# Performance work log

Measured on AMD Instinct MI355X. Metric: run time of the kernel, lower is better.

## Reference

```python
import jax, jax.numpy as jnp
import numpy as np

B, S, C = 4, 4096, 1024   # batch, input_size (seq len), channels
H, D, DK = 16, 64, 256    # nhead, head dim, dim_k (Linformer projection)


def setup_inputs() -> dict:
    key = jax.random.key(0)
    ks = jax.random.split(key, 9)
    s_in = 1.0 / np.sqrt(C)
    s_e = 1.0 / np.sqrt(S)
    return {
        'x':   jax.random.normal(ks[0], (B, S, C), jnp.float32),
        # per-head Q/K/V projection weights (Linear(channels, dim, bias=False))
        'Wq':  jax.random.normal(ks[1], (H, D, C), jnp.float32) * s_in,
        'Wk':  jax.random.normal(ks[2], (H, D, C), jnp.float32) * s_in,
        'Wv':  jax.random.normal(ks[3], (H, D, C), jnp.float32) * s_in,
        # shared (layerwise) E/F Linear(input_size, dim_k) with bias
        'E_w': jax.random.normal(ks[4], (DK, S), jnp.float32) * s_e,
        'E_b': jnp.zeros((DK,), jnp.float32),
        'F_w': jax.random.normal(ks[5], (DK, S), jnp.float32) * s_e,
        'F_b': jnp.zeros((DK,), jnp.float32),
        # output projection Linear(dim*nhead, channels)
        'Wo':  jax.random.normal(ks[6], (C, H * D), jnp.float32) * (1.0 / np.sqrt(H * D)),
        'bo':  jnp.zeros((C,), jnp.float32),
    }


def reference(x, Wq, Wk, Wv, E_w, E_b, F_w, F_b, Wo, bo):
    b, s, c = x.shape
    h, d, _ = Wq.shape
    # per-head projections (vectorized over the Python head loop)
    Q = jnp.einsum('bsc,hdc->bhsd', x, Wq)            # [B,H,S,D]
    Kt = jnp.einsum('bsc,hdc->bhds', x, Wk)           # K already transposed: [B,H,D,S]
    Vt = jnp.einsum('bsc,hdc->bhds', x, Wv)           # [B,H,D,S]
    # Linformer low-rank projections along the sequence axis
    Kp = jnp.einsum('bhds,ks->bhdk', Kt, E_w) + E_b   # [B,H,D,DK]
    Vp = jnp.einsum('bhds,ks->bhdk', Vt, F_w) + F_b   # [B,H,D,DK]
    scores = jnp.einsum('bhsd,bhdk->bhsk', Q, Kp) / jnp.sqrt(jnp.asarray(d, x.dtype))
    P = jax.nn.softmax(scores, axis=-1)               # softmax over projected dim_k
    head_out = jnp.einsum('bhsk,bhdk->bhsd', P, Vp)   # [B,H,S,D]
    out = head_out.transpose(0, 2, 1, 3).reshape(b, s, h * d)  # concat heads
    return out @ Wo.T + bo
```

## Files before the change

kernel.cpp:

```cpp
#include <hip/hip_runtime.h>
#include <stdint.h>

typedef __attribute__((ext_vector_type(8))) short bf16x8;
typedef __attribute__((ext_vector_type(4))) float f32x4;
typedef __attribute__((ext_vector_type(16))) float f32x16;

__device__ __forceinline__ unsigned short f2b(float f) {
  union { float f; uint32_t u; } v; v.f = f;
  uint32_t u = v.u;
  return (unsigned short)((u + 0x7FFFu + ((u >> 16) & 1u)) >> 16);
}

__device__ __forceinline__ void gll16(const unsigned short* gsrc, unsigned short* lds_uniform) {
  __builtin_amdgcn_global_load_lds(
      (const __attribute__((address_space(1))) uint32_t*)gsrc,
      (__attribute__((address_space(3))) uint32_t*)lds_uniform,
      16, 0, 0);
}

#define MFMA(a, b, c) __builtin_amdgcn_mfma_f32_16x16x32_bf16((a), (b), (c), 0, 0, 0)
#define MFMA32(a, b, c) __builtin_amdgcn_mfma_f32_32x32x16_bf16((a), (b), (c), 0, 0, 0)

__global__ void cast_x_dual(const float* __restrict__ x,
                            unsigned short* __restrict__ xb,
                            unsigned short* __restrict__ xT) {
  __shared__ unsigned short tile[64][65];
  const int st = blockIdx.x * 64;
  const int ct = blockIdx.y * 64;
  const int b = blockIdx.z;
  const int t = threadIdx.x;
#pragma unroll
  for (int it = 0; it < 4; ++it) {
    int linear = (it * 256 + t) * 4;
    int r = linear >> 6, c = linear & 63;
    float4 v = *(const float4*)(x + ((size_t)(b * 4096 + st + r)) * 1024 + ct + c);
    ushort4 o;
    o.x = f2b(v.x); o.y = f2b(v.y); o.z = f2b(v.z); o.w = f2b(v.w);
    *(ushort4*)(xb + ((size_t)(b * 4096 + st + r)) * 1024 + ct + c) = o;
    tile[r][c] = o.x; tile[r][c + 1] = o.y; tile[r][c + 2] = o.z; tile[r][c + 3] = o.w;
  }
  __syncthreads();
#pragma unroll
  for (int it = 0; it < 4; ++it) {
    int linear = (it * 256 + t) * 4;
    int r = linear >> 6, c = linear & 63;
    ushort4 o;
    o.x = tile[c][r]; o.y = tile[c + 1][r]; o.z = tile[c + 2][r]; o.w = tile[c + 3][r];
    *(ushort4*)(xT + ((size_t)b * 1024 + ct + r) * 4096 + st + c) = o;
  }
}

__global__ void cast6(const float* __restrict__ s0, const float* __restrict__ s1,
                      const float* __restrict__ s2, const float* __restrict__ s3,
                      const float* __restrict__ s4, const float* __restrict__ s5,
                      const float* __restrict__ E_b, const float* __restrict__ F_b,
                      unsigned short* __restrict__ d0, unsigned short* __restrict__ d1,
                      unsigned short* __restrict__ d2, unsigned short* __restrict__ d3,
                      unsigned short* __restrict__ d4, unsigned short* __restrict__ d5,
                      float* __restrict__ EFbias) {
  if (blockIdx.y == 6) {
    if (blockIdx.x == 0) {
      int t = threadIdx.x;
      EFbias[t] = E_b[t];
      EFbias[256 + t] = F_b[t];
    }
    return;
  }
  const float* src; unsigned short* dst; float sc = 1.0f;
  switch (blockIdx.y) {
    case 0: src = s0; dst = d0; sc = 0.18033688011112042f; break;
    case 1: src = s1; dst = d1; break;
    case 2: src = s2; dst = d2; break;
    case 3: src = s3; dst = d3; break;
    case 4: src = s4; dst = d4; break;
    default: src = s5; dst = d5; break;
  }
  int i = (blockIdx.x * 256 + threadIdx.x) * 4;
  float4 v = *(const float4*)(src + i);
  ushort4 o;
  o.x = f2b(v.x * sc); o.y = f2b(v.y * sc); o.z = f2b(v.z * sc); o.w = f2b(v.w * sc);
  *(ushort4*)(dst + i) = o;
}

template <int BIAS, bool OBF16>
__global__ __launch_bounds__(512, 2) void gemm_bt256(
    const unsigned short* __restrict__ A, const unsigned short* __restrict__ B,
    void* __restrict__ Cout, const float* __restrict__ bias,
    int K, int lda, int ldb, int ldc) {
  __shared__ unsigned short Asm_[2][2][256 * 32];
  __shared__ unsigned short Bsm_[2][2][256 * 32];
  const int tid = threadIdx.x;
  const int wave = tid >> 6, lane = tid & 63;
  const int g = (lane >> 4) & 3, l15 = lane & 15;
  const int wmi = wave >> 2, wni = wave & 3;
  const int bm = blockIdx.x * 256, bn = blockIdx.y * 256;

  const int rc = lane >> 2;

#define STG256(XA, H, J, T, BUF)                                              \
  {                                                                           \
    int k2_ = wave * 2 + (J);                                                 \
    int p_ = k2_ >> 3, cc_ = k2_ & 7;                                         \
    int rr_ = (H) * 128 + cc_ * 16 + rc;                                      \
    int sl_ = (lane & 3) ^ ((rr_ >> 1) & 3);                                  \
    const unsigned short* s_ = (XA)                                           \
        ? A + (size_t)(bm + rr_) * lda + (T) * 64 + p_ * 32 + sl_ * 8         \
        : B + (size_t)(bn + rr_) * ldb + (T) * 64 + p_ * 32 + sl_ * 8;        \
    unsigned short* d_ = ((XA) ? &Asm_[BUF][p_][0] : &Bsm_[BUF][p_][0])       \
                         + ((H) * 128 + cc_ * 16) * 32;                       \
    gll16(s_, d_);                                                            \
  }

  f32x4 acc[8][4];
#pragma unroll
  for (int i = 0; i < 8; ++i)
#pragma unroll
    for (int j = 0; j < 4; ++j) acc[i][j] = (f32x4){0.f, 0.f, 0.f, 0.f};

  const int nt = K >> 6;
  STG256(1, 0, 0, 0, 0) STG256(1, 0, 1, 0, 0)
  STG256(0, 0, 0, 0, 0) STG256(0, 0, 1, 0, 0)
  STG256(1, 1, 0, 0, 0) STG256(1, 1, 1, 0, 0)
  STG256(0, 1, 0, 0, 0) STG256(0, 1, 1, 0, 0)
  asm volatile("s_waitcnt vmcnt(0)" ::: "memory");
  __builtin_amdgcn_s_barrier();
  asm volatile("" ::: "memory");

  for (int t = 0; t < nt; ++t) {
    const int cur = t & 1, nxt = cur ^ 1;
    const char* Ap0 = (const char*)&Asm_[cur][0][0];
    const char* Ap1 = (const char*)&Asm_[cur][1][0];
    const char* Bp0 = (const char*)&Bsm_[cur][0][0];
    const char* Bp1 = (const char*)&Bsm_[cur][1][0];
    const bool more = (t + 1 < nt);

    bf16x8 bf[4][2];
#pragma unroll
    for (int ni = 0; ni < 4; ++ni) {
      int n = wni * 64 + ni * 16 + l15;
      int sw = ((g ^ ((n >> 1) & 3)) << 4);
      bf[ni][0] = *(const bf16x8*)(Bp0 + n * 64 + sw);
      bf[ni][1] = *(const bf16x8*)(Bp1 + n * 64 + sw);
    }

#pragma unroll
    for (int q = 0; q < 4; ++q) {
      if (q == 0 && more) {
        STG256(1, 0, 0, t + 1, nxt) STG256(1, 0, 1, t + 1, nxt)
        STG256(0, 0, 0, t + 1, nxt) STG256(0, 0, 1, t + 1, nxt)
      }
      if (q == 1 && more) {
        STG256(1, 1, 0, t + 1, nxt) STG256(1, 1, 1, t + 1, nxt)
        STG256(0, 1, 0, t + 1, nxt) STG256(0, 1, 1, t + 1, nxt)
      }
      bf16x8 af[2][2];
#pragma unroll
      for (int mi2 = 0; mi2 < 2; ++mi2) {
        int m = wmi * 128 + (q * 2 + mi2) * 16 + l15;
        int sw = ((g ^ ((m >> 1) & 3)) << 4);
        af[mi2][0] = *(const bf16x8*)(Ap0 + m * 64 + sw);
        af[mi2][1] = *(const bf16x8*)(Ap1 + m * 64 + sw);
      }
      __builtin_amdgcn_s_setprio(1);
#pragma unroll
      for (int mi2 = 0; mi2 < 2; ++mi2)
#pragma unroll
        for (int ni = 0; ni < 4; ++ni) {
          acc[q * 2 + mi2][ni] = MFMA(af[mi2][0], bf[ni][0], acc[q * 2 + mi2][ni]);
          acc[q * 2 + mi2][ni] = MFMA(af[mi2][1], bf[ni][1], acc[q * 2 + mi2][ni]);
        }
      __builtin_amdgcn_s_setprio(0);
    }

    asm volatile("s_waitcnt vmcnt(0)" ::: "memory");
    __builtin_amdgcn_s_barrier();
    asm volatile("" ::: "memory");
  }
#undef STG256

#pragma unroll
  for (int mf = 0; mf < 8; ++mf)
#pragma unroll
    for (int r = 0; r < 4; ++r) {
      int row = bm + wmi * 128 + mf * 16 + g * 4 + r;
      float rb = (BIAS == 1) ? bias[row] : 0.f;
#pragma unroll
      for (int ni = 0; ni < 4; ++ni) {
        int col = bn + wni * 64 + ni * 16 + l15;
        float v = acc[mf][ni][r] + rb + ((BIAS == 2) ? bias[col] : 0.f);
        if (OBF16) ((unsigned short*)Cout)[(size_t)row * ldc + col] = f2b(v);
        else       ((float*)Cout)[(size_t)row * ldc + col] = v;
      }
    }
}

__global__ __launch_bounds__(256, 2) void gemm_xef_splitk(
    const unsigned short* __restrict__ A,
    const unsigned short* __restrict__ B,
    float* __restrict__ Cpart) {
  __shared__ unsigned short Asm_[2][128 * 32];
  __shared__ unsigned short Bsm_[2][128 * 32];
  const int tid = threadIdx.x;
  const int wave = tid >> 6, lane = tid & 63;
  const int g = lane >> 4, l15 = lane & 15;
  const int bm = blockIdx.x * 128, bn = blockIdx.y * 128;
  const int z = blockIdx.z, split = z >> 2, b = z & 3;
  const unsigned short* Ab = A + split * 1024;
  const unsigned short* Bb = B + (size_t)b * 1024 * 4096 + split * 1024;
  const int wm = (wave >> 1) * 64, wn = (wave & 1) * 64;

  const int rr0 = wave * 16 + (lane >> 2);
  const int rr1 = rr0 + 64;
  const int sl0 = (lane & 3) ^ ((rr0 >> 1) & 3);
  const int sl1 = (lane & 3) ^ ((rr1 >> 1) & 3);

#define XEF_STAGE(T, BUF)                                                           \
  {                                                                                 \
    int kt_ = (T) * 32;                                                             \
    gll16(Ab + (size_t)(bm + rr0) * 4096 + kt_ + sl0 * 8, Asm_[BUF] + wave * 512);  \
    gll16(Bb + (size_t)(bn + rr0) * 4096 + kt_ + sl0 * 8, Bsm_[BUF] + wave * 512);  \
    gll16(Ab + (size_t)(bm + rr1) * 4096 + kt_ + sl1 * 8, Asm_[BUF] + (wave + 4) * 512); \
    gll16(Bb + (size_t)(bn + rr1) * 4096 + kt_ + sl1 * 8, Bsm_[BUF] + (wave + 4) * 512); \
  }

  f32x4 acc[4][4];
#pragma unroll
  for (int i = 0; i < 4; ++i)
#pragma unroll
    for (int j = 0; j < 4; ++j) acc[i][j] = (f32x4){0.f, 0.f, 0.f, 0.f};

  const int nt = 32;
  XEF_STAGE(0, 0);
  for (int t = 0; t < nt; ++t) {
    const int cur = t & 1;
    if (t + 1 < nt) {
      XEF_STAGE(t + 1, cur ^ 1);
      asm volatile("s_waitcnt vmcnt(4)" ::: "memory");
    } else {
      asm volatile("s_waitcnt vmcnt(0)" ::: "memory");
    }
    __builtin_amdgcn_s_barrier();
    asm volatile("" ::: "memory");

    bf16x8 af[4], bfr[4];
    const char* Ac = (const char*)Asm_[cur];
    const char* Bc = (const char*)Bsm_[cur];
#pragma unroll
    for (int mi = 0; mi < 4; ++mi) {
      int m = wm + mi * 16 + l15;
      af[mi] = *(const bf16x8*)(Ac + m * 64 + ((g ^ ((m >> 1) & 3)) << 4));
    }
#pragma unroll
    for (int ni = 0; ni < 4; ++ni) {
      int n = wn + ni * 16 + l15;
      bfr[ni] = *(const bf16x8*)(Bc + n * 64 + ((g ^ ((n >> 1) & 3)) << 4));
    }
#pragma unroll
    for (int mi = 0; mi < 4; ++mi)
#pragma unroll
      for (int ni = 0; ni < 4; ++ni)
        acc[mi][ni] = MFMA(af[mi], bfr[ni], acc[mi][ni]);

    asm volatile("" ::: "memory");
    __builtin_amdgcn_s_barrier();
  }
#undef XEF_STAGE

  float* C = Cpart + (size_t)z * (512 * 1024);
#pragma unroll
  for (int mi = 0; mi < 4; ++mi)
#pragma unroll
    for (int r = 0; r < 4; ++r) {
      int row = bm + wm + mi * 16 + g * 4 + r;
#pragma unroll
      for (int ni = 0; ni < 4; ++ni) {
        int col = bn + wn + ni * 16 + l15;
        C[(size_t)row * 1024 + col] = acc[mi][ni][r];
      }
    }
}

__global__ void reduce_xef(const float* __restrict__ P,
                           const float* __restrict__ bias,
                           unsigned short* __restrict__ out) {
  int t = blockIdx.x * 256 + threadIdx.x;
  size_t flat = (size_t)t * 4;
  float4 s = *(const float4*)(P + flat);
#pragma unroll
  for (int sp = 1; sp < 4; ++sp) {
    float4 v = *(const float4*)(P + (size_t)sp * 2097152 + flat);
    s.x += v.x; s.y += v.y; s.z += v.z; s.w += v.w;
  }
  float rb = bias[(flat >> 10) & 511];
  ushort4 o;
  o.x = f2b(s.x + rb); o.y = f2b(s.y + rb);
  o.z = f2b(s.z + rb); o.w = f2b(s.w + rb);
  *(ushort4*)(out + flat) = o;
}

template <int BIAS, bool OBF16, int CMODE>
__global__ __launch_bounds__(256, 4) void gemm_bt64(
    const unsigned short* __restrict__ A, const unsigned short* __restrict__ B,
    void* __restrict__ Cout, const float* __restrict__ bias,
    int M, int N, int K, int lda, int ldb, int ldc,
    long long sA, long long sB, long long sC) {
  __shared__ unsigned short Asm_[2][64 * 32];
  __shared__ unsigned short Bsm_[2][64 * 32];
  const int tid = threadIdx.x;
  const int wave = tid >> 6, lane = tid & 63;
  const int g = lane >> 4, l15 = lane & 15;
  const int bm = blockIdx.x * 64, bn = blockIdx.y * 64;
  const unsigned short* Ab = A + (size_t)blockIdx.z * sA;
  const unsigned short* Bb = B + (size_t)blockIdx.z * sB;
  const int wm = (wave >> 1) * 32, wn = (wave & 1) * 32;

  const int rr = wave * 16 + (lane >> 2);
  const int sl = (lane & 3) ^ ((rr >> 1) & 3);

#define BT64_STAGE(T, BUF)                                                      \
  {                                                                             \
    int kt_ = (T) * 32;                                                         \
    gll16(Ab + (size_t)(bm + rr) * lda + kt_ + sl * 8, Asm_[BUF] + wave * 512); \
    gll16(Bb + (size_t)(bn + rr) * ldb + kt_ + sl * 8, Bsm_[BUF] + wave * 512); \
  }

  f32x4 acc[2][2];
#pragma unroll
  for (int i = 0; i < 2; ++i)
#pragma unroll
    for (int j = 0; j < 2; ++j) acc[i][j] = (f32x4){0.f, 0.f, 0.f, 0.f};

  const int nt = K >> 5;
  BT64_STAGE(0, 0);
  for (int t = 0; t < nt; ++t) {
    const int cur = t & 1;
    if (t + 1 < nt) {
      BT64_STAGE(t + 1, cur ^ 1);
      asm volatile("s_waitcnt vmcnt(2)" ::: "memory");
    } else {
      asm volatile("s_waitcnt vmcnt(0)" ::: "memory");
    }
    __builtin_amdgcn_s_barrier();
    asm volatile("" ::: "memory");

    bf16x8 af[2], bfr[2];
    const char* Ac = (const char*)Asm_[cur];
    const char* Bc = (const char*)Bsm_[cur];
#pragma unroll
    for (int mi = 0; mi < 2; ++mi) {
      int m = wm + mi * 16 + l15;
      af[mi] = *(const bf16x8*)(Ac + m * 64 + ((g ^ ((m >> 1) & 3)) << 4));
    }
#pragma unroll
    for (int ni = 0; ni < 2; ++ni) {
      int n = wn + ni * 16 + l15;
      bfr[ni] = *(const bf16x8*)(Bc + n * 64 + ((g ^ ((n >> 1) & 3)) << 4));
    }
#pragma unroll
    for (int mi = 0; mi < 2; ++mi)
#pragma unroll
      for (int ni = 0; ni < 2; ++ni)
        acc[mi][ni] = MFMA(af[mi], bfr[ni], acc[mi][ni]);

    asm volatile("" ::: "memory");
    __builtin_amdgcn_s_barrier();
  }
#undef BT64_STAGE

#pragma unroll
  for (int mi = 0; mi < 2; ++mi)
#pragma unroll
    for (int r = 0; r < 4; ++r) {
      int row = bm + wm + mi * 16 + g * 4 + r;
      float rb = (BIAS == 1) ? bias[row] : 0.f;
#pragma unroll
      for (int ni = 0; ni < 2; ++ni) {
        int col = bn + wn + ni * 16 + l15;
        float v = acc[mi][ni][r] + rb + ((BIAS == 2) ? bias[col] : 0.f);
        size_t idx;
        if (CMODE == 1) {
          idx = (size_t)(col >> 6) * ((size_t)M * 64) + (size_t)row * 64 + (col & 63);
        } else if (CMODE == 2) {
          int cl = col & 15;
          int cp = (cl & 3) | ((cl & 4) << 1) | ((cl & 8) >> 1);
          idx = (size_t)row * ldc + (col & ~15) + cp;
        } else {
          idx = (size_t)row * ldc + col;
        }
        if (OBF16) ((unsigned short*)Cout + (size_t)blockIdx.z * sC)[idx] = f2b(v);
        else       ((float*)Cout + (size_t)blockIdx.z * sC)[idx] = v;
      }
    }
}

__global__ __launch_bounds__(256, 4) void attn_kernel(
    const unsigned short* __restrict__ q,
    const unsigned short* __restrict__ kp,
    const unsigned short* __restrict__ vp,
    unsigned short* __restrict__ ho) {
  __shared__ unsigned short Ksm[256 * 64];
  __shared__ float Lsm[4 * 32];

  const int tid = threadIdx.x;
  const int wave = tid >> 6, lane = tid & 63;
  const int l31 = lane & 31, hi = lane >> 5;
  const int x = blockIdx.x;
  const int bh = (x & 7) + ((x >> 8) << 3);
  const int qq = (x >> 3) & 31;
  const int b = bh >> 4, h = bh & 15;
  const int s0 = qq * 128;

  const unsigned short* kph = kp + (size_t)bh * (256 * 64);
  const unsigned short* vph = vp + (size_t)bh * (64 * 256);

  {
    const int r = (lane >> 3), sl = (lane & 7) ^ (lane >> 3);
#pragma unroll
    for (int it = 0; it < 8; ++it) {
      int c = it * 4 + wave;
      gll16(kph + (c * 8 + r) * 64 + sl * 8, Ksm + c * 512);
    }
  }

  const int srow = s0 + wave * 32 + l31;
  const unsigned short* qrow = q + (size_t)(b * 4096 + srow) * 1024 + h * 64;
  bf16x8 qf[4];
#pragma unroll
  for (int dc = 0; dc < 4; ++dc)
    qf[dc] = *(const bf16x8*)(qrow + dc * 16 + hi * 8);

  __syncthreads();

  f32x16 ho0 = {0,0,0,0,0,0,0,0,0,0,0,0,0,0,0,0};
  f32x16 ho1 = {0,0,0,0,0,0,0,0,0,0,0,0,0,0,0,0};
  float sum = 0.f;

#pragma unroll
  for (int t = 0; t < 8; ++t) {
    bf16x8 vf00 = *(const bf16x8*)(vph + (size_t)l31 * 256 + (t * 2 + 0) * 16 + hi * 8);
    bf16x8 vf01 = *(const bf16x8*)(vph + (size_t)l31 * 256 + (t * 2 + 1) * 16 + hi * 8);
    bf16x8 vf10 = *(const bf16x8*)(vph + (size_t)(32 + l31) * 256 + (t * 2 + 0) * 16 + hi * 8);
    bf16x8 vf11 = *(const bf16x8*)(vph + (size_t)(32 + l31) * 256 + (t * 2 + 1) * 16 + hi * 8);

    f32x16 qk = {0,0,0,0,0,0,0,0,0,0,0,0,0,0,0,0};
    const int krow = t * 32 + l31;
    const char* kbase = (const char*)Ksm + krow * 128;
#pragma unroll
    for (int dc = 0; dc < 4; ++dc) {
      bf16x8 kf = *(const bf16x8*)(kbase + (((dc * 2 + hi) ^ (l31 & 7)) << 4));
      qk = MFMA32(kf, qf[dc], qk);
    }

    uint32_t pk[8];
#pragma unroll
    for (int j = 0; j < 8; ++j) {
      float e0 = exp2f(qk[2 * j]);
      float e1 = exp2f(qk[2 * j + 1]);
      sum += e0 + e1;
      asm("v_cvt_pk_bf16_f32 %0, %1, %2" : "=v"(pk[j]) : "v"(e0), "v"(e1));
    }
    union { uint32_t u[4]; bf16x8 v; } ua, ub;
    ua.u[0] = pk[0]; ua.u[1] = pk[1]; ua.u[2] = pk[2]; ua.u[3] = pk[3];
    ub.u[0] = pk[4]; ub.u[1] = pk[5]; ub.u[2] = pk[6]; ub.u[3] = pk[7];

    ho0 = MFMA32(ua.v, vf00, ho0);
    ho0 = MFMA32(ub.v, vf01, ho0);
    ho1 = MFMA32(ua.v, vf10, ho1);
    ho1 = MFMA32(ub.v, vf11, ho1);
  }

  sum += __shfl_xor(sum, 32);
  if (lane < 32) Lsm[wave * 32 + lane] = sum;

  float rl[16];
#pragma unroll
  for (int g = 0; g < 4; ++g) {
    float4 d4 = *(const float4*)&Lsm[wave * 32 + g * 8 + hi * 4];
    rl[g * 4 + 0] = __builtin_amdgcn_rcpf(d4.x);
    rl[g * 4 + 1] = __builtin_amdgcn_rcpf(d4.y);
    rl[g * 4 + 2] = __builtin_amdgcn_rcpf(d4.z);
    rl[g * 4 + 3] = __builtin_amdgcn_rcpf(d4.w);
  }

  unsigned short* hob = ho + (size_t)(b * 4096 + s0 + wave * 32) * 1024 + h * 64 + l31;
#pragma unroll
  for (int reg = 0; reg < 16; ++reg) {
    int srw = (reg & 3) + 8 * (reg >> 2) + 4 * hi;
    hob[(size_t)srw * 1024]      = f2b(ho0[reg] * rl[reg]);
    hob[(size_t)srw * 1024 + 32] = f2b(ho1[reg] * rl[reg]);
  }
}

extern "C" void kernel_launch(void* const* d_in, const int* in_sizes, int n_in,
                              void* d_out, int out_size, void* d_ws, size_t ws_size,
                              hipStream_t stream) {
  (void)in_sizes; (void)n_in; (void)out_size; (void)ws_size;
  const float* x   = (const float*)d_in[0];
  const float* Wq  = (const float*)d_in[1];
  const float* Wk  = (const float*)d_in[2];
  const float* Wv  = (const float*)d_in[3];
  const float* E_w = (const float*)d_in[4];
  const float* E_b = (const float*)d_in[5];
  const float* F_w = (const float*)d_in[6];
  const float* F_b = (const float*)d_in[7];
  const float* Wo  = (const float*)d_in[8];
  const float* bo  = (const float*)d_in[9];
  float* out = (float*)d_out;

  char* ws = (char*)d_ws;
  unsigned short* xb   = (unsigned short*)(ws);
  unsigned short* xT   = (unsigned short*)(ws + 33554432);
  unsigned short* Qb   = (unsigned short*)(ws + 67108864);
  unsigned short* Wqb  = (unsigned short*)(ws + 100663296);
  unsigned short* Wkb  = (unsigned short*)(ws + 102760448);
  unsigned short* Wvb  = (unsigned short*)(ws + 104857600);
  unsigned short* Wob  = (unsigned short*)(ws + 106954752);
  unsigned short* EFb  = (unsigned short*)(ws + 109051904);
  unsigned short* xEF  = (unsigned short*)(ws + 113246208);
  unsigned short* Kp   = (unsigned short*)(ws + 117440512);
  unsigned short* Vp   = (unsigned short*)(ws + 119537664);
  float*          EFbias = (float*)(ws + 121634816);
  float*          Ppart  = (float*)(ws + 121700352);
  unsigned short* HO   = xb;

  cast_x_dual<<<dim3(64, 16, 4), 256, 0, stream>>>(x, xb, xT);
  cast6<<<dim3(1024, 7), 256, 0, stream>>>(
      Wq, Wk, Wv, E_w, F_w, Wo, E_b, F_b,
      Wqb, Wkb, Wvb, EFb, EFb + 2097152 / 2, Wob, EFbias);

  gemm_bt256<0, true><<<dim3(64, 4), 512, 0, stream>>>(
      xb, Wqb, Qb, nullptr, 1024, 1024, 1024, 1024);

  gemm_xef_splitk<<<dim3(4, 8, 16), 256, 0, stream>>>(EFb, xT, Ppart);
  reduce_xef<<<dim3(2048, 1, 1), 256, 0, stream>>>(Ppart, EFbias, xEF);

  gemm_bt64<0, true, 1><<<dim3(4, 16, 4), 256, 0, stream>>>(
      xEF, Wkb, Kp, nullptr, 256, 1024, 1024, 1024, 1024, 1024,
      512LL * 1024, 0LL, 256LL * 1024);

  gemm_bt64<0, true, 2><<<dim3(16, 4, 4), 256, 0, stream>>>(
      Wvb, xEF + 256 * 1024, Vp, nullptr, 1024, 256, 1024, 1024, 1024, 256,
      0LL, 512LL * 1024, 1024LL * 256);

  attn_kernel<<<dim3(2048, 1, 1), 256, 0, stream>>>(Qb, Kp, Vp, HO);

  gemm_bt256<2, false><<<dim3(64, 4), 512, 0, stream>>>(
      HO, Wob, out, bo, 1024, 1024, 1024, 1024);
}
```

Baseline: 224.0 us.

## Use triple-buffered K=32 LDS pipeline with prefetch distance two in gemm_bt256

The 256x256 GEMM kernel now works on K=32 slices held in three LDS buffers instead of two double-buffered K=64 slices. Loads are issued two iterations ahead and waited on with vmcnt(4), so one K-slice of global loads stays in flight across the barrier. The aim is to hide global-load latency better and to simplify the fragment loads and MFMA loop. In exchange there are twice as many barriers per unit of K, and launch_bounds drops to 1 block per CU, which may reduce occupancy.

```diff
diff --git a/kernel.cpp b/kernel.cpp
--- a/kernel.cpp
+++ b/kernel.cpp
@@ -83,32 +83,31 @@
 }
 
 template <int BIAS, bool OBF16>
-__global__ __launch_bounds__(512, 2) void gemm_bt256(
+__global__ __launch_bounds__(512, 1) void gemm_bt256(
     const unsigned short* __restrict__ A, const unsigned short* __restrict__ B,
     void* __restrict__ Cout, const float* __restrict__ bias,
     int K, int lda, int ldb, int ldc) {
-  __shared__ unsigned short Asm_[2][2][256 * 32];
-  __shared__ unsigned short Bsm_[2][2][256 * 32];
+  __shared__ unsigned short Asm_[3][256 * 32];
+  __shared__ unsigned short Bsm_[3][256 * 32];
   const int tid = threadIdx.x;
   const int wave = tid >> 6, lane = tid & 63;
   const int g = (lane >> 4) & 3, l15 = lane & 15;
   const int wmi = wave >> 2, wni = wave & 3;
   const int bm = blockIdx.x * 256, bn = blockIdx.y * 256;
 
-  const int rc = lane >> 2;
-
-#define STG256(XA, H, J, T, BUF)                                              \
-  {                                                                           \
-    int k2_ = wave * 2 + (J);                                                 \
-    int p_ = k2_ >> 3, cc_ = k2_ & 7;                                         \
-    int rr_ = (H) * 128 + cc_ * 16 + rc;                                      \
-    int sl_ = (lane & 3) ^ ((rr_ >> 1) & 3);                                  \
-    const unsigned short* s_ = (XA)                                           \
-        ? A + (size_t)(bm + rr_) * lda + (T) * 64 + p_ * 32 + sl_ * 8         \
-        : B + (size_t)(bn + rr_) * ldb + (T) * 64 + p_ * 32 + sl_ * 8;        \
-    unsigned short* d_ = ((XA) ? &Asm_[BUF][p_][0] : &Bsm_[BUF][p_][0])       \
-                         + ((H) * 128 + cc_ * 16) * 32;                       \
-    gll16(s_, d_);                                                            \
+  const int c0 = wave * 2;
+  const int rr0 = c0 * 16 + (lane >> 2);
+  const int rr1 = rr0 + 16;
+  const int sl0 = (lane & 3) ^ ((rr0 >> 1) & 3);
+  const int sl1 = (lane & 3) ^ ((rr1 >> 1) & 3);
+
+#define STG(T, BUF)                                                                   \
+  {                                                                                   \
+    int kt_ = (T) * 32;                                                               \
+    gll16(A + (size_t)(bm + rr0) * lda + kt_ + sl0 * 8, Asm_[BUF] + c0 * 512);        \
+    gll16(B + (size_t)(bn + rr0) * ldb + kt_ + sl0 * 8, Bsm_[BUF] + c0 * 512);        \
+    gll16(A + (size_t)(bm + rr1) * lda + kt_ + sl1 * 8, Asm_[BUF] + (c0 + 1) * 512);  \
+    gll16(B + (size_t)(bn + rr1) * ldb + kt_ + sl1 * 8, Bsm_[BUF] + (c0 + 1) * 512);  \
   }
 
   f32x4 acc[8][4];
@@ -117,66 +116,46 @@
 #pragma unroll
     for (int j = 0; j < 4; ++j) acc[i][j] = (f32x4){0.f, 0.f, 0.f, 0.f};
 
-  const int nt = K >> 6;
-  STG256(1, 0, 0, 0, 0) STG256(1, 0, 1, 0, 0)
-  STG256(0, 0, 0, 0, 0) STG256(0, 0, 1, 0, 0)
-  STG256(1, 1, 0, 0, 0) STG256(1, 1, 1, 0, 0)
-  STG256(0, 1, 0, 0, 0) STG256(0, 1, 1, 0, 0)
-  asm volatile("s_waitcnt vmcnt(0)" ::: "memory");
+  const int nt = K >> 5;
+  STG(0, 0);
+  STG(1, 1);
+  asm volatile("s_waitcnt vmcnt(4)" ::: "memory");
   __builtin_amdgcn_s_barrier();
   asm volatile("" ::: "memory");
 
   for (int t = 0; t < nt; ++t) {
-    const int cur = t & 1, nxt = cur ^ 1;
-    const char* Ap0 = (const char*)&Asm_[cur][0][0];
-    const char* Ap1 = (const char*)&Asm_[cur][1][0];
-    const char* Bp0 = (const char*)&Bsm_[cur][0][0];
-    const char* Bp1 = (const char*)&Bsm_[cur][1][0];
-    const bool more = (t + 1 < nt);
-
-    bf16x8 bf[4][2];
-#pragma unroll
-    for (int ni = 0; ni < 4; ++ni) {
-      int n = wni * 64 + ni * 16 + l15;
-      int sw = ((g ^ ((n >> 1) & 3)) << 4);
-      bf[ni][0] = *(const bf16x8*)(Bp0 + n * 64 + sw);
-      bf[ni][1] = *(const bf16x8*)(Bp1 + n * 64 + sw);
-    }
-
-#pragma unroll
-    for (int q = 0; q < 4; ++q) {
-      if (q == 0 && more) {
-        STG256(1, 0, 0, t + 1, nxt) STG256(1, 0, 1, t + 1, nxt)
-        STG256(0, 0, 0, t + 1, nxt) STG256(0, 0, 1, t + 1, nxt)
-      }
-      if (q == 1 && more) {
-        STG256(1, 1, 0, t + 1, nxt) STG256(1, 1, 1, t + 1, nxt)
-        STG256(0, 1, 0, t + 1, nxt) STG256(0, 1, 1, t + 1, nxt)
-      }
-      bf16x8 af[2][2];
-#pragma unroll
-      for (int mi2 = 0; mi2 < 2; ++mi2) {
-        int m = wmi * 128 + (q * 2 + mi2) * 16 + l15;
-        int sw = ((g ^ ((m >> 1) & 3)) << 4);
-        af[mi2][0] = *(const bf16x8*)(Ap0 + m * 64 + sw);
-        af[mi2][1] = *(const bf16x8*)(Ap1 + m * 64 + sw);
-      }
-      __builtin_amdgcn_s_setprio(1);
-#pragma unroll
-      for (int mi2 = 0; mi2 < 2; ++mi2)
-#pragma unroll
-        for (int ni = 0; ni < 4; ++ni) {
-          acc[q * 2 + mi2][ni] = MFMA(af[mi2][0], bf[ni][0], acc[q * 2 + mi2][ni]);
-          acc[q * 2 + mi2][ni] = MFMA(af[mi2][1], bf[ni][1], acc[q * 2 + mi2][ni]);
-        }
-      __builtin_amdgcn_s_setprio(0);
-    }
-
-    asm volatile("s_waitcnt vmcnt(0)" ::: "memory");
+    const int cur = t % 3;
+    const char* Ac = (const char*)Asm_[cur];
+    const char* Bc = (const char*)Bsm_[cur];
+
+    bf16x8 afr[8], bfr[4];
+#pragma unroll
+    for (int mf = 0; mf < 8; ++mf) {
+      int m = wmi * 128 + mf * 16 + l15;
+      afr[mf] = *(const bf16x8*)(Ac + m * 64 + ((g ^ ((m >> 1) & 3)) << 4));
+    }
+#pragma unroll
+    for (int nf = 0; nf < 4; ++nf) {
+      int n = wni * 64 + nf * 16 + l15;
+      bfr[nf] = *(const bf16x8*)(Bc + n * 64 + ((g ^ ((n >> 1) & 3)) << 4));
+    }
+
+    if (t + 2 < nt) STG(t + 2, (t + 2) % 3);
+
+    __builtin_amdgcn_s_setprio(1);
+#pragma unroll
+    for (int mf = 0; mf < 8; ++mf)
+#pragma unroll
+      for (int nf = 0; nf < 4; ++nf)
+        acc[mf][nf] = MFMA(afr[mf], bfr[nf], acc[mf][nf]);
+    __builtin_amdgcn_s_setprio(0);
+
+    if (t + 2 < nt) asm volatile("s_waitcnt vmcnt(4)" ::: "memory");
+    else            asm volatile("s_waitcnt vmcnt(0)" ::: "memory");
     __builtin_amdgcn_s_barrier();
     asm volatile("" ::: "memory");
   }
-#undef STG256
+#undef STG
 
 #pragma unroll
   for (int mf = 0; mf < 8; ++mf)
@@ -185,9 +164,9 @@
       int row = bm + wmi * 128 + mf * 16 + g * 4 + r;
       float rb = (BIAS == 1) ? bias[row] : 0.f;
 #pragma unroll
-      for (int ni = 0; ni < 4; ++ni) {
-        int col = bn + wni * 64 + ni * 16 + l15;
-        float v = acc[mf][ni][r] + rb + ((BIAS == 2) ? bias[col] : 0.f);
+      for (int nf = 0; nf < 4; ++nf) {
+        int col = bn + wni * 64 + nf * 16 + l15;
+        float v = acc[mf][nf][r] + rb + ((BIAS == 2) ? bias[col] : 0.f);
         if (OBF16) ((unsigned short*)Cout)[(size_t)row * ldc + col] = f2b(v);
         else       ((float*)Cout)[(size_t)row * ldc + col] = v;
       }
```

New measurement: 213.1 us. 4.9% less time.
